# Kernel tuning notes

Measured on AMD Instinct MI355X. Metric: run time of the kernel, lower is better.

## Reference

```python
import jax, jax.numpy as jnp
import numpy as np

N, E, F_IN, H, O = 50000, 800000, 128, 8, 8  # nodes, edges, in_feat, heads, out-per-head
NEG_SLOPE = 0.2

def setup_inputs() -> dict:
    key = jax.random.key(0)
    k1, k2, k3, k4, k5, k6 = jax.random.split(key, 6)
    h = jax.random.normal(k1, (N, F_IN), dtype=jnp.float32)
    # xavier_uniform-like scale (gain=1.414) expressed via normal init scale
    w_scale = 1.414 * np.sqrt(2.0 / (F_IN + O)).astype(np.float32)
    W = jax.random.normal(k2, (H, F_IN, O), dtype=jnp.float32) * w_scale
    a_scale = 1.414 * np.sqrt(2.0 / (2 * O + 1)).astype(np.float32)
    a1 = jax.random.normal(k3, (H, O), dtype=jnp.float32) * a_scale
    a2 = jax.random.normal(k4, (H, O), dtype=jnp.float32) * a_scale
    src = jax.random.randint(k5, (E,), 0, N, dtype=jnp.int64 if jax.config.jax_enable_x64 else jnp.int32)
    dst = jax.random.randint(k6, (E,), 0, N, dtype=jnp.int64 if jax.config.jax_enable_x64 else jnp.int32)
    return {"h": h, "W": W, "a1": a1, "a2": a2, "src": src, "dst": dst}

def reference(h, W, a1, a2, src, dst):
    # Per-head linear projection: [N, H, O]
    Wh = jnp.einsum('nf,hfo->nho', h, W)
    # Per-node attention half-scores (a split into src/dst halves): [N, H]
    s_src = jnp.einsum('nho,ho->nh', Wh, a1)
    s_dst = jnp.einsum('nho,ho->nh', Wh, a2)
    # Edge attention logits: [E, H]
    e = jax.nn.leaky_relu(s_src[src] + s_dst[dst], negative_slope=NEG_SLOPE)
    # Numerically-stable segment softmax over incoming edges of each dst node
    m = jax.ops.segment_max(e, dst, num_segments=N)          # [N, H]
    m = jnp.where(jnp.isfinite(m), m, jnp.float32(0.0))      # isolated nodes -> 0
    p = jnp.exp(e - m[dst])                                   # [E, H]
    denom = jax.ops.segment_sum(p, dst, num_segments=N)       # [N, H]
    attn = p / jnp.maximum(denom[dst], jnp.float32(1e-16))    # [E, H]
    # Weighted scatter-sum of messages: [N, H, O]
    out = jax.ops.segment_sum(attn[:, :, None] * Wh[src], dst, num_segments=N)
    # Concatenate heads: [N, H*O]
    return out.reshape(N, H * O)
```

## Files before the change

### kernel.cpp

```cpp
#include <hip/hip_runtime.h>
#include <hip/hip_bf16.h>
#include <hip/hip_fp16.h>


#define FIN 128
#define NH 8
#define NO 8
#define NC 64
#define GR 64
#define EPB 4096
#define BCAP 8192

typedef __attribute__((ext_vector_type(8))) short bf16x8;
typedef __attribute__((ext_vector_type(4))) float f32x4;

static __device__ __forceinline__ unsigned short f2bf(float f) {
    unsigned u = __float_as_uint(f);
    u += 0x7fff + ((u >> 16) & 1);
    return (unsigned short)(u >> 16);
}

__global__ __launch_bounds__(256) void gemm_s_scat_kernel(
    const float* __restrict__ h, const float* __restrict__ W,
    const float* __restrict__ a1, const float* __restrict__ a2,
    const int* __restrict__ src, const int* __restrict__ dst,
    int* __restrict__ bcnt, unsigned* __restrict__ packed,
    __half* __restrict__ Wh, float* __restrict__ s_src, float* __restrict__ s_dst,
    int N, int E, int gemm_blocks)
{
    __shared__ unsigned short hA[GR * FIN];
    __shared__ unsigned short wB[NC * FIN];
    const int tid = threadIdx.x;

    if (blockIdx.x >= gemm_blocks) {
        int* cnt_l  = (int*)hA;
        int* base_l = cnt_l + 256;
        const long e0 = (long)(blockIdx.x - gemm_blocks) * EPB;
        cnt_l[tid] = 0;
        __syncthreads();
        int br[16];
        unsigned pk[16];
#pragma unroll
        for (int j = 0; j < 16; ++j) {
            long e = e0 + j * 256 + tid;
            bool ok = (e < E);
            int d = ok ? dst[e] : 0;
            int s = ok ? src[e] : 0;
            int b = d >> 8;
            int r = ok ? atomicAdd(&cnt_l[b], 1) : 0;
            br[j] = ok ? ((b << 16) | r) : -1;
            pk[j] = ((unsigned)(d & 255) << 16) | (unsigned)s;
        }
        __syncthreads();
        if (cnt_l[tid] > 0) base_l[tid] = atomicAdd(&bcnt[tid], cnt_l[tid]);
        __syncthreads();
#pragma unroll
        for (int j = 0; j < 16; ++j) {
            if (br[j] >= 0) {
                int b = br[j] >> 16, r = br[j] & 0xFFFF;
                packed[(long)b * BCAP + base_l[b] + r] = pk[j];
            }
        }
        return;
    }

    const int row0 = blockIdx.x * GR;
    {
        int r = tid >> 2;
        int c0 = (tid & 3) * 32;
        int n = row0 + r;
        const float4* hp = (const float4*)(h + (long)n * FIN + c0);
        char* basep = (char*)hA + r * (FIN * 2);
        int sw = (r & 7) << 4;
#pragma unroll
        for (int j = 0; j < 8; ++j) {
            float4 v = (n < N) ? hp[j] : make_float4(0.f, 0.f, 0.f, 0.f);
            ushort4 b;
            b.x = f2bf(v.x); b.y = f2bf(v.y); b.z = f2bf(v.z); b.w = f2bf(v.w);
            int byte = (c0 + j * 4) * 2;
            *(ushort4*)(basep + (byte ^ sw)) = b;
        }
    }
    for (int i = tid; i < NH * FIN * NO; i += 256) {
        int hh = i >> 10, f = (i >> 3) & 127, o = i & 7;
        int c = hh * 8 + o;
        *(unsigned short*)((char*)wB + c * (FIN * 2) + ((f * 2) ^ ((c & 7) << 4))) = f2bf(W[i]);
    }
    __syncthreads();

    const int w    = tid >> 6;
    const int lane = tid & 63;
    const int l15  = lane & 15;
    const int lg   = lane >> 4;
    const int arow = w * 16 + l15;

    f32x4 acc[4] = {{0,0,0,0},{0,0,0,0},{0,0,0,0},{0,0,0,0}};
    const char* hbase = (const char*)hA + arow * (FIN * 2);
    const int hsw = (arow & 7) << 4;
#pragma unroll
    for (int kk = 0; kk < 4; ++kk) {
        int kb = kk * 64 + lg * 16;
        bf16x8 af = *(const bf16x8*)(hbase + (kb ^ hsw));
#pragma unroll
        for (int nt = 0; nt < 4; ++nt) {
            int c = nt * 16 + l15;
            bf16x8 bf = *(const bf16x8*)((const char*)wB + c * (FIN * 2) + (kb ^ ((c & 7) << 4)));
            acc[nt] = __builtin_amdgcn_mfma_f32_16x16x32_bf16(af, bf, acc[nt], 0, 0, 0);
        }
    }

#pragma unroll
    for (int nt = 0; nt < 4; ++nt) {
        int col = nt * 16 + l15;
        float a1c = a1[col];
        float a2c = a2[col];
#pragma unroll
        for (int r = 0; r < 4; ++r) {
            int n = row0 + w * 16 + lg * 4 + r;
            float v = acc[nt][r];
            bool ok = (n < N);
            if (ok) Wh[(long)n * NC + col] = __float2half_rn(v);
            float ps = v * a1c, pd = v * a2c;
            ps += __shfl_xor(ps, 1); pd += __shfl_xor(pd, 1);
            ps += __shfl_xor(ps, 2); pd += __shfl_xor(pd, 2);
            ps += __shfl_xor(ps, 4); pd += __shfl_xor(pd, 4);
            if (ok && (col & 7) == 0) {
                s_src[n * NH + (col >> 3)] = ps;
                s_dst[n * NH + (col >> 3)] = pd;
            }
        }
    }
}

__global__ __launch_bounds__(256) void bucketB_kernel(
    const unsigned* __restrict__ packed, const int* __restrict__ bcnt,
    int* __restrict__ row_off, unsigned short* __restrict__ srcs,
    int N, int E, int nb)
{
    __shared__ int bins[256];
    __shared__ int scan_s[256];
    __shared__ int g0s;
    __shared__ unsigned short outb[BCAP];
    const int t = threadIdx.x;
    const int b = blockIdx.x;
    const int d0 = b << 8;
    const unsigned* pin = packed + (long)b * BCAP;

    int v2 = (t < nb) ? bcnt[t] : 0;
    scan_s[t] = v2;
    __syncthreads();
    for (int off = 1; off < 256; off <<= 1) {
        int u = (t >= off) ? scan_s[t - off] : 0;
        __syncthreads();
        scan_s[t] += u;
        __syncthreads();
    }
    if (t == b) g0s = scan_s[t] - v2;
    bins[t] = 0;
    __syncthreads();
    const int g0 = g0s;
    const int cnt = bcnt[b];

    for (int i = t; i < cnt; i += 256)
        atomicAdd(&bins[pin[i] >> 16], 1);
    __syncthreads();
    int v = bins[t];
    scan_s[t] = v;
    __syncthreads();
    for (int off = 1; off < 256; off <<= 1) {
        int u = (t >= off) ? scan_s[t - off] : 0;
        __syncthreads();
        scan_s[t] += u;
        __syncthreads();
    }
    if (d0 + t < N) row_off[d0 + t] = g0 + scan_s[t] - v;
    if (b == nb - 1 && t == 0) row_off[N] = E;
    bins[t] = scan_s[t] - v;
    __syncthreads();
    for (int i = t; i < cnt; i += 256) {
        unsigned p = pin[i];
        int pos = atomicAdd(&bins[p >> 16], 1);
        outb[pos] = (unsigned short)(p & 0xFFFF);
    }
    __syncthreads();
    for (int i = t; i < cnt; i += 256)
        srcs[g0 + i] = outb[i];
}

__global__ __launch_bounds__(256) void gather_kernel(
    const unsigned short* __restrict__ srcs, const int* __restrict__ row_off,
    const float* __restrict__ s_src, const float* __restrict__ s_dst,
    const __half* __restrict__ Wh, float* __restrict__ out, int N)
{
    int wid = blockIdx.x * 4 + (threadIdx.x >> 6);
    if (wid >= N) return;
    const int lane = threadIdx.x & 63;
    const int el = lane >> 3;
    const int hh = lane & 7;
    int beg = row_off[wid];
    int end = row_off[wid + 1];
    float sd = s_dst[wid * NH + hh];
    float acc = 0.f, den = 0.f;

    for (int i = beg; i < end; i += 8) {
        int idx = i + el;
        bool val = (idx < end);
        int s = (int)srcs[val ? idx : beg];
        float ss = s_src[s * NH + hh];
        float x = ss + sd;
        x = (x > 0.f) ? x : 0.2f * x;
        float p = __expf(x);
        p = val ? p : 0.f;
        den += p;
#pragma unroll
        for (int k = 0; k < 8; ++k) {
            int sk   = __shfl(s, k * 8);
            float pk = __shfl(p, k * 8 + (lane >> 3));
            float wv = __half2float(Wh[((unsigned)sk << 6) | (unsigned)lane]);
            acc = fmaf(pk, wv, acc);
        }
    }
    den += __shfl_xor(den, 8);
    den += __shfl_xor(den, 16);
    den += __shfl_xor(den, 32);
    float den_b = __shfl(den, lane >> 3);
    out[(unsigned)wid * NC + (unsigned)lane] = acc / fmaxf(den_b, 1e-16f);
}

extern "C" void kernel_launch(void* const* d_in, const int* in_sizes, int n_in,
                              void* d_out, int out_size, void* d_ws, size_t ws_size,
                              hipStream_t stream)
{
    const float* h  = (const float*)d_in[0];
    const float* W  = (const float*)d_in[1];
    const float* a1 = (const float*)d_in[2];
    const float* a2 = (const float*)d_in[3];
    const int*  src = (const int*)d_in[4];
    const int*  dst = (const int*)d_in[5];
    float* out = (float*)d_out;

    const int N = in_sizes[0] / FIN;
    const int E = in_sizes[4];
    const int nb = (N + 255) >> 8;

    char* wsb = (char*)d_ws;
    __half* Wh         = (__half*)wsb;           wsb += (size_t)N * NC * 2;
    float* s_src       = (float*)wsb;            wsb += (size_t)N * NH * 4;
    float* s_dst       = (float*)wsb;            wsb += (size_t)N * NH * 4;
    int* row_off       = (int*)wsb;              wsb += (size_t)(N + 1) * 4;
    int* bcnt          = (int*)wsb;              wsb += (size_t)256 * 4;
    unsigned* packed   = (unsigned*)wsb;         wsb += (size_t)nb * BCAP * 4;
    unsigned short* srcs = (unsigned short*)wsb; wsb += (size_t)E * 2;

    hipMemsetAsync(bcnt, 0, 256 * 4, stream);

    const int gemm_blocks = (N + GR - 1) / GR;
    const int scat_blocks = (E + EPB - 1) / EPB;
    gemm_s_scat_kernel<<<gemm_blocks + scat_blocks, 256, 0, stream>>>(
        h, W, a1, a2, src, dst, bcnt, packed, Wh, s_src, s_dst, N, E, gemm_blocks);

    bucketB_kernel<<<nb, 256, 0, stream>>>(packed, bcnt, row_off, srcs, N, E, nb);

    int g_blocks = (N + 3) / 4;
    gather_kernel<<<g_blocks, 256, 0, stream>>>(srcs, row_off, s_src, s_dst, Wh, out, N);
}
```

Baseline: 74.28 us.

## Fold attention vectors into extra GEMM columns and prebuild bf16 weight tile

A one-block prep kernel converts W to swizzled bf16 once and appends 16 extra columns holding W·a1 and W·a2 per head, so the attention half-scores come straight out of a fifth MFMA tile instead of shuffle reductions. Each GEMM block now copies the prebuilt weight tile with vector loads rather than re-converting W from fp32. The prep kernel also zeroes the bucket counters, replacing the memset. The cost is one more MFMA tile per k-step, a larger shared weight buffer, and bf16 rounding of the folded vectors, which slightly changes score precision.

```diff
diff --git a/kernel.cpp b/kernel.cpp
--- a/kernel.cpp
+++ b/kernel.cpp
@@ -7,6 +7,7 @@
 #define NH 8
 #define NO 8
 #define NC 64
+#define NB_COLS 80
 #define GR 64
 #define EPB 4096
 #define BCAP 8192
@@ -20,16 +21,40 @@
     return (unsigned short)(u >> 16);
 }
 
+__global__ __launch_bounds__(256) void prep_kernel(
+    const float* __restrict__ W, const float* __restrict__ a1, const float* __restrict__ a2,
+    unsigned short* __restrict__ wBg, int* __restrict__ bcnt)
+{
+    const int t = threadIdx.x;
+    bcnt[t] = 0;
+    for (int i = t; i < NH * FIN * NO; i += 256) {
+        int hh = i >> 10, f = (i >> 3) & 127, o = i & 7;
+        int c = hh * 8 + o;
+        wBg[c * FIN + (f ^ ((c & 7) << 3))] = f2bf(W[i]);
+    }
+    for (int i = t; i < 16 * FIN; i += 256) {
+        int j = i >> 7;
+        int f = i & 127;
+        int hh = j & 7;
+        const float* av = (j < 8) ? (a1 + hh * NO) : (a2 + (hh)*NO);
+        const float* wv = W + hh * (FIN * NO) + f * NO;
+        float s = 0.f;
+#pragma unroll
+        for (int o = 0; o < 8; ++o) s += wv[o] * av[o];
+        int c = 64 + j;
+        wBg[c * FIN + (f ^ ((c & 7) << 3))] = f2bf(s);
+    }
+}
+
 __global__ __launch_bounds__(256) void gemm_s_scat_kernel(
-    const float* __restrict__ h, const float* __restrict__ W,
-    const float* __restrict__ a1, const float* __restrict__ a2,
+    const float* __restrict__ h, const unsigned short* __restrict__ wBg,
     const int* __restrict__ src, const int* __restrict__ dst,
     int* __restrict__ bcnt, unsigned* __restrict__ packed,
     __half* __restrict__ Wh, float* __restrict__ s_src, float* __restrict__ s_dst,
     int N, int E, int gemm_blocks)
 {
-    __shared__ unsigned short hA[GR * FIN];
-    __shared__ unsigned short wB[NC * FIN];
+    __shared__ alignas(16) unsigned short hA[GR * FIN];
+    __shared__ alignas(16) unsigned short wB[NB_COLS * FIN];
     const int tid = threadIdx.x;
 
     if (blockIdx.x >= gemm_blocks) {
@@ -81,10 +106,12 @@
             *(ushort4*)(basep + (byte ^ sw)) = b;
         }
     }
-    for (int i = tid; i < NH * FIN * NO; i += 256) {
-        int hh = i >> 10, f = (i >> 3) & 127, o = i & 7;
-        int c = hh * 8 + o;
-        *(unsigned short*)((char*)wB + c * (FIN * 2) + ((f * 2) ^ ((c & 7) << 4))) = f2bf(W[i]);
+    {
+        const uint4* s4 = (const uint4*)wBg;
+        uint4* d4 = (uint4*)wB;
+#pragma unroll
+        for (int j = 0; j < 5; ++j)
+            d4[j * 256 + tid] = s4[j * 256 + tid];
     }
     __syncthreads();
 
@@ -94,7 +121,7 @@
     const int lg   = lane >> 4;
     const int arow = w * 16 + l15;
 
-    f32x4 acc[4] = {{0,0,0,0},{0,0,0,0},{0,0,0,0},{0,0,0,0}};
+    f32x4 acc[5] = {{0,0,0,0},{0,0,0,0},{0,0,0,0},{0,0,0,0},{0,0,0,0}};
     const char* hbase = (const char*)hA + arow * (FIN * 2);
     const int hsw = (arow & 7) << 4;
 #pragma unroll
@@ -102,7 +129,7 @@
         int kb = kk * 64 + lg * 16;
         bf16x8 af = *(const bf16x8*)(hbase + (kb ^ hsw));
 #pragma unroll
-        for (int nt = 0; nt < 4; ++nt) {
+        for (int nt = 0; nt < 5; ++nt) {
             int c = nt * 16 + l15;
             bf16x8 bf = *(const bf16x8*)((const char*)wB + c * (FIN * 2) + (kb ^ ((c & 7) << 4)));
             acc[nt] = __builtin_amdgcn_mfma_f32_16x16x32_bf16(af, bf, acc[nt], 0, 0, 0);
@@ -112,22 +139,19 @@
 #pragma unroll
     for (int nt = 0; nt < 4; ++nt) {
         int col = nt * 16 + l15;
-        float a1c = a1[col];
-        float a2c = a2[col];
 #pragma unroll
         for (int r = 0; r < 4; ++r) {
             int n = row0 + w * 16 + lg * 4 + r;
-            float v = acc[nt][r];
-            bool ok = (n < N);
-            if (ok) Wh[(long)n * NC + col] = __float2half_rn(v);
-            float ps = v * a1c, pd = v * a2c;
-            ps += __shfl_xor(ps, 1); pd += __shfl_xor(pd, 1);
-            ps += __shfl_xor(ps, 2); pd += __shfl_xor(pd, 2);
-            ps += __shfl_xor(ps, 4); pd += __shfl_xor(pd, 4);
-            if (ok && (col & 7) == 0) {
-                s_src[n * NH + (col >> 3)] = ps;
-                s_dst[n * NH + (col >> 3)] = pd;
-            }
+            if (n < N) Wh[(long)n * NC + col] = __float2half_rn(acc[nt][r]);
+        }
+    }
+#pragma unroll
+    for (int r = 0; r < 4; ++r) {
+        int n = row0 + w * 16 + lg * 4 + r;
+        if (n < N) {
+            float v = acc[4][r];
+            if (l15 < 8) s_src[n * NH + l15] = v;
+            else         s_dst[n * NH + (l15 - 8)] = v;
         }
     }
 }
@@ -249,15 +273,16 @@
     float* s_dst       = (float*)wsb;            wsb += (size_t)N * NH * 4;
     int* row_off       = (int*)wsb;              wsb += (size_t)(N + 1) * 4;
     int* bcnt          = (int*)wsb;              wsb += (size_t)256 * 4;
+    unsigned short* wBg = (unsigned short*)wsb;  wsb += (size_t)NB_COLS * FIN * 2;
     unsigned* packed   = (unsigned*)wsb;         wsb += (size_t)nb * BCAP * 4;
     unsigned short* srcs = (unsigned short*)wsb; wsb += (size_t)E * 2;
 
-    hipMemsetAsync(bcnt, 0, 256 * 4, stream);
+    prep_kernel<<<1, 256, 0, stream>>>(W, a1, a2, wBg, bcnt);
 
     const int gemm_blocks = (N + GR - 1) / GR;
     const int scat_blocks = (E + EPB - 1) / EPB;
     gemm_s_scat_kernel<<<gemm_blocks + scat_blocks, 256, 0, stream>>>(
-        h, W, a1, a2, src, dst, bcnt, packed, Wh, s_src, s_dst, N, E, gemm_blocks);
+        h, wBg, src, dst, bcnt, packed, Wh, s_src, s_dst, N, E, gemm_blocks);
 
     bucketB_kernel<<<nb, 256, 0, stream>>>(packed, bcnt, row_off, srcs, N, E, nb);
 
```

Measured after the change: 72.85 us. Within noise of the previous version (-1.9%).
